# Performance work log

Measured on AMD Instinct MI355X. Metric: run time of the kernel, lower is better.

Reference implementation:

```python
import jax, jax.numpy as jnp
import numpy as np

N_NODES = 50000
N_EDGES = 400000
D_IN = 512
D_OUT = 512


def setup_inputs() -> dict:
    key = jax.random.key(0)
    k1, k2, k3, k4, k5 = jax.random.split(key, 5)
    x = jax.random.normal(k1, (N_NODES, D_IN), dtype=jnp.float32)
    adj_rows = jax.random.randint(k2, (N_EDGES,), 0, N_NODES, dtype=jnp.int32)
    adj_cols = jax.random.randint(k3, (N_EDGES,), 0, N_NODES, dtype=jnp.int32)
    adj_vals = jax.random.uniform(k4, (N_EDGES,), dtype=jnp.float32)
    # Xavier uniform init for weight, zeros for bias (as in reset_parameters)
    limit = float(np.sqrt(6.0 / (D_IN + D_OUT)))
    weight = jax.random.uniform(k5, (D_IN, D_OUT), minval=-limit, maxval=limit, dtype=jnp.float32)
    bias = jnp.zeros((D_OUT,), dtype=jnp.float32)
    return {"x": x, "adj_rows": adj_rows, "adj_cols": adj_cols,
            "adj_vals": adj_vals, "weight": weight, "bias": bias}


def reference(x, adj_rows, adj_cols, adj_vals, weight, bias):
    # support = x @ W  : dense GEMM [N, D_in] x [D_in, D_out]
    support = jnp.matmul(x, weight)
    # output = spmm(adj, support): COO sparse-dense matmul via gather + segment_sum
    messages = adj_vals[:, None] * support[adj_cols]  # [E, D_out]
    output = jax.ops.segment_sum(messages, adj_rows, num_segments=N_NODES)
    return output + bias
```

## Files before the change

kernel.cpp:

```cpp
#include <hip/hip_runtime.h>

#define N_NODES 50000
#define N_EDGES 400000
#define DIM 512
#define NPAD 50048
#define MTILES 391
#define NTILES 4

typedef short  short8  __attribute__((ext_vector_type(8)));
typedef unsigned short ushort8 __attribute__((ext_vector_type(8)));
typedef float  f32x4   __attribute__((ext_vector_type(4)));
typedef int    int2v   __attribute__((ext_vector_type(2)));

typedef __attribute__((address_space(1))) const unsigned short gu16;
typedef __attribute__((address_space(3))) unsigned short lu16;

__device__ __forceinline__ unsigned short f2bf(float f) {
    unsigned int u = __float_as_uint(f);
    u += 0x7fffu + ((u >> 16) & 1u);
    return (unsigned short)(u >> 16);
}
__device__ __forceinline__ float bf2f(unsigned short h) {
    return __uint_as_float(((unsigned int)h) << 16);
}

__global__ __launch_bounds__(256) void cast_x_kernel(const float* __restrict__ x,
                                                     unsigned short* __restrict__ xb) {
    size_t t = (size_t)blockIdx.x * 256 + threadIdx.x;
    size_t base = t * 8;
    int row = (int)(base >> 9);
    ushort8 o;
    if (row < N_NODES) {
        f32x4 a = *(const f32x4*)(x + base);
        f32x4 b = *(const f32x4*)(x + base + 4);
        o[0] = f2bf(a[0]); o[1] = f2bf(a[1]); o[2] = f2bf(a[2]); o[3] = f2bf(a[3]);
        o[4] = f2bf(b[0]); o[5] = f2bf(b[1]); o[6] = f2bf(b[2]); o[7] = f2bf(b[3]);
    } else {
        #pragma unroll
        for (int q = 0; q < 8; ++q) o[q] = 0;
    }
    *(ushort8*)(xb + base) = o;
}

__global__ __launch_bounds__(256) void cast_wt_kernel(const float* __restrict__ w,
                                                      unsigned short* __restrict__ wt) {
    int t = blockIdx.x * 256 + threadIdx.x;
    int n = t >> 9, k = t & 511;
    wt[t] = f2bf(w[k * 512 + n]);
}

__global__ __launch_bounds__(256) void hist_kernel(const int* __restrict__ rows,
                                                   int* __restrict__ counts) {
    int e = blockIdx.x * 256 + threadIdx.x;
    if (e < N_EDGES) atomicAdd(&counts[rows[e]], 1);
}

__global__ __launch_bounds__(512) void scan_blocks_kernel(const int* __restrict__ counts,
                                                          int* __restrict__ tmp,
                                                          int* __restrict__ partials) {
    __shared__ int sm[512];
    int i = blockIdx.x * 512 + threadIdx.x;
    int v = (i < N_NODES) ? counts[i] : 0;
    sm[threadIdx.x] = v;
    __syncthreads();
    #pragma unroll
    for (int off = 1; off < 512; off <<= 1) {
        int val = 0;
        if ((int)threadIdx.x >= off) val = sm[threadIdx.x - off];
        __syncthreads();
        if ((int)threadIdx.x >= off) sm[threadIdx.x] += val;
        __syncthreads();
    }
    if (i < N_NODES) tmp[i] = sm[threadIdx.x] - v;
    if (threadIdx.x == 511) partials[blockIdx.x] = sm[511];
}

__global__ __launch_bounds__(128) void scan_partials_kernel(int* __restrict__ partials) {
    __shared__ int sm[128];
    const int nb = 98;
    int v = ((int)threadIdx.x < nb) ? partials[threadIdx.x] : 0;
    sm[threadIdx.x] = v;
    __syncthreads();
    #pragma unroll
    for (int off = 1; off < 128; off <<= 1) {
        int val = 0;
        if ((int)threadIdx.x >= off) val = sm[threadIdx.x - off];
        __syncthreads();
        if ((int)threadIdx.x >= off) sm[threadIdx.x] += val;
        __syncthreads();
    }
    if ((int)threadIdx.x < nb) partials[threadIdx.x] = sm[threadIdx.x] - v;
}

__global__ __launch_bounds__(256) void add_offsets_kernel(const int* __restrict__ tmp,
                                                          const int* __restrict__ partials,
                                                          int* __restrict__ row_start,
                                                          int* __restrict__ cursor) {
    int i = blockIdx.x * 256 + threadIdx.x;
    if (i < N_NODES) {
        int rs = tmp[i] + partials[i >> 9];
        row_start[i] = rs;
        cursor[i] = rs;
    }
}

__global__ __launch_bounds__(256) void scatter_kernel(const int* __restrict__ rows,
                                                      const int* __restrict__ cols,
                                                      const float* __restrict__ vals,
                                                      int* __restrict__ cursor,
                                                      int2v* __restrict__ csr_cv) {
    int e = blockIdx.x * 256 + threadIdx.x;
    if (e < N_EDGES) {
        int r = rows[e];
        int p = atomicAdd(&cursor[r], 1);
        int2v cv;
        cv[0] = cols[e];
        cv[1] = __float_as_int(vals[e]);
        csr_cv[p] = cv;
    }
}

__global__ __launch_bounds__(256) void gemm_kernel(const unsigned short* __restrict__ Xb,
                                                   const unsigned short* __restrict__ Wt,
                                                   unsigned short* __restrict__ S) {
    __shared__ __align__(16) unsigned short As[128 * 32];
    __shared__ __align__(16) unsigned short Bs[128 * 32];
    const int m0 = blockIdx.y * 128;
    const int n0 = blockIdx.x * 128;
    const int t = threadIdx.x;
    const int lane = t & 63;
    const int w = t >> 6;
    const int wr = w >> 1, wc = w & 1;
    const int fr = lane & 15;
    const int kg = lane >> 4;

    f32x4 acc[4][4];
    #pragma unroll
    for (int i = 0; i < 4; ++i)
        #pragma unroll
        for (int j = 0; j < 4; ++j)
            #pragma unroll
            for (int q = 0; q < 4; ++q) acc[i][j][q] = 0.0f;

    const int row0 = w * 16 + (lane >> 2);
    const int row1 = row0 + 64;
    const int col0 = (lane & 3) * 8;
    lu16* AsW = (lu16*)(As + w * 512);
    lu16* BsW = (lu16*)(Bs + w * 512);

    const unsigned short* gA0 = Xb + (size_t)(m0 + row0) * DIM + col0;
    const unsigned short* gA1 = Xb + (size_t)(m0 + row1) * DIM + col0;
    const unsigned short* gB0 = Wt + (size_t)(n0 + row0) * DIM + col0;
    const unsigned short* gB1 = Wt + (size_t)(n0 + row1) * DIM + col0;

    for (int kk = 0; kk < DIM; kk += 32) {
        __builtin_amdgcn_global_load_lds((gu16*)(gA0 + kk), AsW,        16, 0, 0);
        __builtin_amdgcn_global_load_lds((gu16*)(gA1 + kk), AsW + 2048, 16, 0, 0);
        __builtin_amdgcn_global_load_lds((gu16*)(gB0 + kk), BsW,        16, 0, 0);
        __builtin_amdgcn_global_load_lds((gu16*)(gB1 + kk), BsW + 2048, 16, 0, 0);
        __syncthreads();

        short8 af[4], bf[4];
        #pragma unroll
        for (int mi = 0; mi < 4; ++mi)
            af[mi] = *(const short8*)&As[(wr * 64 + mi * 16 + fr) * 32 + kg * 8];
        #pragma unroll
        for (int ni = 0; ni < 4; ++ni)
            bf[ni] = *(const short8*)&Bs[(wc * 64 + ni * 16 + fr) * 32 + kg * 8];

        #pragma unroll
        for (int mi = 0; mi < 4; ++mi)
            #pragma unroll
            for (int ni = 0; ni < 4; ++ni)
                acc[mi][ni] = __builtin_amdgcn_mfma_f32_16x16x32_bf16(af[mi], bf[ni], acc[mi][ni], 0, 0, 0);

        __syncthreads();
    }

    #pragma unroll
    for (int mi = 0; mi < 4; ++mi) {
        #pragma unroll
        for (int ni = 0; ni < 4; ++ni) {
            int gr = m0 + wr * 64 + mi * 16 + kg * 4;
            int gc = n0 + wc * 64 + ni * 16 + fr;
            #pragma unroll
            for (int j = 0; j < 4; ++j)
                S[(size_t)(gr + j) * DIM + gc] = f2bf(acc[mi][ni][j]);
        }
    }
}

__global__ __launch_bounds__(64) void spmm_kernel(const unsigned short* __restrict__ S,
                                                  const int* __restrict__ row_start,
                                                  const int* __restrict__ counts,
                                                  const int2v* __restrict__ cv,
                                                  const float* __restrict__ bias,
                                                  float* __restrict__ out) {
    const int r = blockIdx.x;
    const int lane = threadIdx.x;
    const int s = row_start[r];
    const int n = counts[r];
    const size_t lo = (size_t)lane * 8;

    float acc[8];
    #pragma unroll
    for (int q = 0; q < 8; ++q) acc[q] = 0.0f;

    for (int j = 0; j < n; j += 4) {
        int2v e0 = cv[s + j];
        int2v e1 = cv[s + j + 1];
        int2v e2 = cv[s + j + 2];
        int2v e3 = cv[s + j + 3];
        int c0 = e0[0];
        int c1 = (j + 1 < n) ? e1[0] : 0;
        int c2 = (j + 2 < n) ? e2[0] : 0;
        int c3 = (j + 3 < n) ? e3[0] : 0;
        float v0 = __int_as_float(e0[1]);
        float v1 = (j + 1 < n) ? __int_as_float(e1[1]) : 0.0f;
        float v2 = (j + 2 < n) ? __int_as_float(e2[1]) : 0.0f;
        float v3 = (j + 3 < n) ? __int_as_float(e3[1]) : 0.0f;
        ushort8 x0 = *(const ushort8*)&S[(size_t)c0 * DIM + lo];
        ushort8 x1 = *(const ushort8*)&S[(size_t)c1 * DIM + lo];
        ushort8 x2 = *(const ushort8*)&S[(size_t)c2 * DIM + lo];
        ushort8 x3 = *(const ushort8*)&S[(size_t)c3 * DIM + lo];
        #pragma unroll
        for (int q = 0; q < 8; ++q) {
            acc[q] += v0 * bf2f(x0[q]);
            acc[q] += v1 * bf2f(x1[q]);
            acc[q] += v2 * bf2f(x2[q]);
            acc[q] += v3 * bf2f(x3[q]);
        }
    }

    #pragma unroll
    for (int q = 0; q < 8; ++q) acc[q] += bias[lane * 8 + q];

    f32x4 o0, o1;
    #pragma unroll
    for (int q = 0; q < 4; ++q) { o0[q] = acc[q]; o1[q] = acc[4 + q]; }
    __builtin_nontemporal_store(o0, (f32x4*)&out[(size_t)r * DIM + lo]);
    __builtin_nontemporal_store(o1, (f32x4*)&out[(size_t)r * DIM + lo + 4]);
}

extern "C" void kernel_launch(void* const* d_in, const int* in_sizes, int n_in,
                              void* d_out, int out_size, void* d_ws, size_t ws_size,
                              hipStream_t stream) {
    const float* x    = (const float*)d_in[0];
    const int*   rows = (const int*)d_in[1];
    const int*   cols = (const int*)d_in[2];
    const float* vals = (const float*)d_in[3];
    const float* w    = (const float*)d_in[4];
    const float* bias = (const float*)d_in[5];
    float* out = (float*)d_out;

    char* ws = (char*)d_ws;
    size_t off = 0;
    auto alloc = [&](size_t bytes) -> char* {
        char* p = ws + off;
        off = (off + bytes + 255) & ~(size_t)255;
        return p;
    };
    unsigned short* Xb      = (unsigned short*)alloc((size_t)NPAD * DIM * 2);
    unsigned short* Wt      = (unsigned short*)alloc((size_t)DIM * DIM * 2);
    unsigned short* S       = (unsigned short*)alloc((size_t)NPAD * DIM * 2);
    int*            counts  = (int*)alloc((size_t)N_NODES * 4);
    int*            tmp     = (int*)alloc((size_t)N_NODES * 4);
    int*            rstart  = (int*)alloc((size_t)N_NODES * 4);
    int*            cursor  = (int*)alloc((size_t)N_NODES * 4);
    int*            partials= (int*)alloc(512);
    int2v*          csr_cv  = (int2v*)alloc((size_t)(N_EDGES + 8) * 8);

    hipMemsetAsync(counts, 0, (size_t)N_NODES * 4, stream);

    cast_x_kernel<<<(NPAD * DIM / 8) / 256, 256, 0, stream>>>(x, Xb);
    cast_wt_kernel<<<(DIM * DIM) / 256, 256, 0, stream>>>(w, Wt);

    hist_kernel<<<(N_EDGES + 255) / 256, 256, 0, stream>>>(rows, counts);
    scan_blocks_kernel<<<98, 512, 0, stream>>>(counts, tmp, partials);
    scan_partials_kernel<<<1, 128, 0, stream>>>(partials);
    add_offsets_kernel<<<(N_NODES + 255) / 256, 256, 0, stream>>>(tmp, partials, rstart, cursor);
    scatter_kernel<<<(N_EDGES + 255) / 256, 256, 0, stream>>>(rows, cols, vals, cursor, csr_cv);

    gemm_kernel<<<dim3(NTILES, MTILES), 256, 0, stream>>>(Xb, Wt, S);
    spmm_kernel<<<N_NODES, 64, 0, stream>>>(S, rstart, counts, csr_cv, bias, out);
}
```

Baseline: 353.9 us.

## Widen GEMM K-tile, remap blocks per XCD, fuse weight cast with histogram, batch SpMM rows

```diff
diff --git a/kernel.cpp b/kernel.cpp
--- a/kernel.cpp
+++ b/kernel.cpp
@@ -6,6 +6,7 @@
 #define NPAD 50048
 #define MTILES 391
 #define NTILES 4
+#define NWG (MTILES * NTILES)
 
 typedef short  short8  __attribute__((ext_vector_type(8)));
 typedef unsigned short ushort8 __attribute__((ext_vector_type(8)));
@@ -42,17 +43,19 @@
     *(ushort8*)(xb + base) = o;
 }
 
-__global__ __launch_bounds__(256) void cast_wt_kernel(const float* __restrict__ w,
-                                                      unsigned short* __restrict__ wt) {
-    int t = blockIdx.x * 256 + threadIdx.x;
-    int n = t >> 9, k = t & 511;
-    wt[t] = f2bf(w[k * 512 + n]);
-}
-
-__global__ __launch_bounds__(256) void hist_kernel(const int* __restrict__ rows,
-                                                   int* __restrict__ counts) {
-    int e = blockIdx.x * 256 + threadIdx.x;
-    if (e < N_EDGES) atomicAdd(&counts[rows[e]], 1);
+__global__ __launch_bounds__(256) void wt_hist_kernel(const float* __restrict__ w,
+                                                      unsigned short* __restrict__ wt,
+                                                      const int* __restrict__ rows,
+                                                      int* __restrict__ counts) {
+    int b = blockIdx.x;
+    if (b < 1024) {
+        int t = b * 256 + threadIdx.x;
+        int n = t >> 9, k = t & 511;
+        wt[t] = f2bf(w[k * 512 + n]);
+    } else {
+        int e = (b - 1024) * 256 + threadIdx.x;
+        if (e < N_EDGES) atomicAdd(&counts[rows[e]], 1);
+    }
 }
 
 __global__ __launch_bounds__(512) void scan_blocks_kernel(const int* __restrict__ counts,
@@ -123,10 +126,16 @@
 __global__ __launch_bounds__(256) void gemm_kernel(const unsigned short* __restrict__ Xb,
                                                    const unsigned short* __restrict__ Wt,
                                                    unsigned short* __restrict__ S) {
-    __shared__ __align__(16) unsigned short As[128 * 32];
-    __shared__ __align__(16) unsigned short Bs[128 * 32];
-    const int m0 = blockIdx.y * 128;
-    const int n0 = blockIdx.x * 128;
+    __shared__ __align__(16) unsigned short As[128 * 64];
+    __shared__ __align__(16) unsigned short Bs[128 * 64];
+
+    const int q = NWG / 8, r8 = NWG % 8;
+    int b = blockIdx.x;
+    int xcd = b & 7, loc = b >> 3;
+    int l = (xcd < r8 ? xcd * (q + 1) : r8 * (q + 1) + (xcd - r8) * q) + loc;
+    const int m0 = (l >> 2) * 128;
+    const int n0 = (l & 3) * 128;
+
     const int t = threadIdx.x;
     const int lane = t & 63;
     const int w = t >> 6;
@@ -140,39 +149,42 @@
         #pragma unroll
         for (int j = 0; j < 4; ++j)
             #pragma unroll
-            for (int q = 0; q < 4; ++q) acc[i][j][q] = 0.0f;
-
-    const int row0 = w * 16 + (lane >> 2);
-    const int row1 = row0 + 64;
-    const int col0 = (lane & 3) * 8;
-    lu16* AsW = (lu16*)(As + w * 512);
-    lu16* BsW = (lu16*)(Bs + w * 512);
-
-    const unsigned short* gA0 = Xb + (size_t)(m0 + row0) * DIM + col0;
-    const unsigned short* gA1 = Xb + (size_t)(m0 + row1) * DIM + col0;
-    const unsigned short* gB0 = Wt + (size_t)(n0 + row0) * DIM + col0;
-    const unsigned short* gB1 = Wt + (size_t)(n0 + row1) * DIM + col0;
-
-    for (int kk = 0; kk < DIM; kk += 32) {
-        __builtin_amdgcn_global_load_lds((gu16*)(gA0 + kk), AsW,        16, 0, 0);
-        __builtin_amdgcn_global_load_lds((gu16*)(gA1 + kk), AsW + 2048, 16, 0, 0);
-        __builtin_amdgcn_global_load_lds((gu16*)(gB0 + kk), BsW,        16, 0, 0);
-        __builtin_amdgcn_global_load_lds((gu16*)(gB1 + kk), BsW + 2048, 16, 0, 0);
-        __syncthreads();
-
-        short8 af[4], bf[4];
+            for (int qq = 0; qq < 4; ++qq) acc[i][j][qq] = 0.0f;
+
+    const int srow = w * 8 + (lane >> 3);
+    const int scol = (lane & 7) * 8;
+    const unsigned short* gA = Xb + (size_t)(m0 + srow) * DIM + scol;
+    const unsigned short* gB = Wt + (size_t)(n0 + srow) * DIM + scol;
+    lu16* AsW = (lu16*)As + w * 512;
+    lu16* BsW = (lu16*)Bs + w * 512;
+
+    for (int kk = 0; kk < DIM; kk += 64) {
+        #pragma unroll
+        for (int c = 0; c < 4; ++c) {
+            __builtin_amdgcn_global_load_lds((gu16*)(gA + (size_t)c * 32 * DIM + kk), AsW + c * 2048, 16, 0, 0);
+            __builtin_amdgcn_global_load_lds((gu16*)(gB + (size_t)c * 32 * DIM + kk), BsW + c * 2048, 16, 0, 0);
+        }
+        __syncthreads();
+
+        short8 af[4][2], bf[4][2];
         #pragma unroll
         for (int mi = 0; mi < 4; ++mi)
-            af[mi] = *(const short8*)&As[(wr * 64 + mi * 16 + fr) * 32 + kg * 8];
+            #pragma unroll
+            for (int ks = 0; ks < 2; ++ks)
+                af[mi][ks] = *(const short8*)&As[(wr * 64 + mi * 16 + fr) * 64 + ks * 32 + kg * 8];
         #pragma unroll
         for (int ni = 0; ni < 4; ++ni)
-            bf[ni] = *(const short8*)&Bs[(wc * 64 + ni * 16 + fr) * 32 + kg * 8];
-
-        #pragma unroll
-        for (int mi = 0; mi < 4; ++mi)
-            #pragma unroll
-            for (int ni = 0; ni < 4; ++ni)
-                acc[mi][ni] = __builtin_amdgcn_mfma_f32_16x16x32_bf16(af[mi], bf[ni], acc[mi][ni], 0, 0, 0);
+            #pragma unroll
+            for (int ks = 0; ks < 2; ++ks)
+                bf[ni][ks] = *(const short8*)&Bs[(wc * 64 + ni * 16 + fr) * 64 + ks * 32 + kg * 8];
+
+        #pragma unroll
+        for (int ks = 0; ks < 2; ++ks)
+            #pragma unroll
+            for (int mi = 0; mi < 4; ++mi)
+                #pragma unroll
+                for (int ni = 0; ni < 4; ++ni)
+                    acc[mi][ni] = __builtin_amdgcn_mfma_f32_16x16x32_bf16(af[mi][ks], bf[ni][ks], acc[mi][ni], 0, 0, 0);
 
         __syncthreads();
     }
@@ -190,14 +202,14 @@
     }
 }
 
-__global__ __launch_bounds__(64) void spmm_kernel(const unsigned short* __restrict__ S,
-                                                  const int* __restrict__ row_start,
-                                                  const int* __restrict__ counts,
-                                                  const int2v* __restrict__ cv,
-                                                  const float* __restrict__ bias,
-                                                  float* __restrict__ out) {
-    const int r = blockIdx.x;
-    const int lane = threadIdx.x;
+__global__ __launch_bounds__(256) void spmm_kernel(const unsigned short* __restrict__ S,
+                                                   const int* __restrict__ row_start,
+                                                   const int* __restrict__ counts,
+                                                   const int2v* __restrict__ cv,
+                                                   const float* __restrict__ bias,
+                                                   float* __restrict__ out) {
+    const int r = blockIdx.x * 4 + (threadIdx.x >> 6);
+    const int lane = threadIdx.x & 63;
     const int s = row_start[r];
     const int n = counts[r];
     const size_t lo = (size_t)lane * 8;
@@ -238,8 +250,8 @@
     f32x4 o0, o1;
     #pragma unroll
     for (int q = 0; q < 4; ++q) { o0[q] = acc[q]; o1[q] = acc[4 + q]; }
-    __builtin_nontemporal_store(o0, (f32x4*)&out[(size_t)r * DIM + lo]);
-    __builtin_nontemporal_store(o1, (f32x4*)&out[(size_t)r * DIM + lo + 4]);
+    *(f32x4*)&out[(size_t)r * DIM + lo] = o0;
+    *(f32x4*)&out[(size_t)r * DIM + lo + 4] = o1;
 }
 
 extern "C" void kernel_launch(void* const* d_in, const int* in_sizes, int n_in,
@@ -273,14 +285,13 @@
     hipMemsetAsync(counts, 0, (size_t)N_NODES * 4, stream);
 
     cast_x_kernel<<<(NPAD * DIM / 8) / 256, 256, 0, stream>>>(x, Xb);
-    cast_wt_kernel<<<(DIM * DIM) / 256, 256, 0, stream>>>(w, Wt);
-
-    hist_kernel<<<(N_EDGES + 255) / 256, 256, 0, stream>>>(rows, counts);
+    wt_hist_kernel<<<1024 + (N_EDGES + 255) / 256, 256, 0, stream>>>(w, Wt, rows, counts);
+
     scan_blocks_kernel<<<98, 512, 0, stream>>>(counts, tmp, partials);
     scan_partials_kernel<<<1, 128, 0, stream>>>(partials);
     add_offsets_kernel<<<(N_NODES + 255) / 256, 256, 0, stream>>>(tmp, partials, rstart, cursor);
     scatter_kernel<<<(N_EDGES + 255) / 256, 256, 0, stream>>>(rows, cols, vals, cursor, csr_cv);
 
-    gemm_kernel<<<dim3(NTILES, MTILES), 256, 0, stream>>>(Xb, Wt, S);
-    spmm_kernel<<<N_NODES, 64, 0, stream>>>(S, rstart, counts, csr_cv, bias, out);
-}
+    gemm_kernel<<<NWG, 256, 0, stream>>>(Xb, Wt, S);
+    spmm_kernel<<<N_NODES / 4, 256, 0, stream>>>(S, rstart, counts, csr_cv, bias, out);
+}
```

New measurement: 348.1 us. About the same (-1.6%).
